# Performance work log

Hardware: AMD Instinct MI355X
Metric: run time of the kernel (lower is better)

The kernel has to match this reference:

```python
import jax, jax.numpy as jnp
import numpy as np

B, L, E, H = 2, 2048, 1024, 16
D = E // H
EPS = 1e-5


def setup_inputs() -> dict:
    key = jax.random.key(0)
    ks = jax.random.split(key, 12)
    s = 1.0 / np.sqrt(E)
    x = jax.random.normal(ks[0], (B, L, E), dtype=jnp.float32)
    # bool mask: True = block. Causal upper-triangular mask (L, S) with S == L.
    mask = jnp.triu(jnp.ones((L, L), dtype=jnp.bool_), k=1)
    Wq = jax.random.normal(ks[1], (E, E), jnp.float32) * s
    bq = jax.random.normal(ks[2], (E,), jnp.float32) * 0.01
    Wk = jax.random.normal(ks[3], (E, E), jnp.float32) * s
    bk = jax.random.normal(ks[4], (E,), jnp.float32) * 0.01
    Wv = jax.random.normal(ks[5], (E, E), jnp.float32) * s
    bv = jax.random.normal(ks[6], (E,), jnp.float32) * 0.01
    Wo = jax.random.normal(ks[7], (E, E), jnp.float32) * s
    bo = jax.random.normal(ks[8], (E,), jnp.float32) * 0.01
    gamma = jnp.ones((E,), jnp.float32)
    beta = jnp.zeros((E,), jnp.float32)
    return {"x": x, "mask": mask, "Wq": Wq, "bq": bq, "Wk": Wk, "bk": bk,
            "Wv": Wv, "bv": bv, "Wo": Wo, "bo": bo, "gamma": gamma, "beta": beta}


def reference(x, mask, Wq, bq, Wk, bk, Wv, bv, Wo, bo, gamma, beta):
    b, l, e = x.shape
    x = jnp.nan_to_num(x, nan=0.0, posinf=1e9, neginf=-1e9)
    # QKV projections (torch Linear: x @ W.T + b), split heads -> (B,H,L,D)
    q = (x @ Wq.T + bq).reshape(b, l, H, D).transpose(0, 2, 1, 3)
    k = (x @ Wk.T + bk).reshape(b, l, H, D).transpose(0, 2, 1, 3)
    v = (x @ Wv.T + bv).reshape(b, l, H, D).transpose(0, 2, 1, 3)
    scale = max(D ** 0.5, 1e-6)
    scores = jnp.einsum('bhtd,bhsd->bhts', q, k) / scale  # (B,H,L,L)
    # bool mask True=block -> additive -inf, broadcast (L,L) over (B,H)
    scores = scores + jnp.where(mask, -jnp.inf, 0.0).astype(scores.dtype)
    scores = scores - jnp.max(scores, axis=-1, keepdims=True)
    scores = jnp.nan_to_num(scores, nan=0.0, posinf=1e9, neginf=-1e9)
    attn = jax.nn.softmax(scores, axis=-1)
    o = jnp.einsum('bhts,bhsd->bhtd', attn, v)
    o = o.transpose(0, 2, 1, 3).reshape(b, l, e)
    y = o @ Wo.T + bo
    r = y + x
    # LayerNorm over last dim
    mu = jnp.mean(r, axis=-1, keepdims=True)
    var = jnp.mean((r - mu) ** 2, axis=-1, keepdims=True)
    out = (r - mu) * jax.lax.rsqrt(var + EPS) * gamma + beta
    out = jnp.nan_to_num(out, nan=0.0, posinf=1e9, neginf=-1e9)
    return out
```

## Files before the change

### kernel.cpp

```cpp
#include <hip/hip_runtime.h>
#include <hip/hip_bf16.h>
#include <cstdint>
#include <cstddef>

#define NB 2
#define NL 2048
#define NE 1024
#define NH 16
#define ND 64
#define NM (NB * NL)

typedef float f32x4 __attribute__((ext_vector_type(4)));
typedef __bf16 bf16x8 __attribute__((ext_vector_type(8)));
typedef __bf16 bf16x4 __attribute__((ext_vector_type(4)));

#define DEV static __device__ __forceinline__

DEV f32x4 mfma16(bf16x8 a, bf16x8 b, f32x4 c) {
  return __builtin_amdgcn_mfma_f32_16x16x32_bf16(a, b, c, 0, 0, 0);
}

DEV ushort f2bf(float f) {
  uint32_t u = __float_as_uint(f);
  uint32_t r = (u + 0x7fffu + ((u >> 16) & 1u)) >> 16;
  return (ushort)r;
}

#if __has_builtin(__builtin_amdgcn_exp2f)
DEV float fast_exp2(float x) { return __builtin_amdgcn_exp2f(x); }
#else
DEV float fast_exp2(float x) { return exp2f(x); }
#endif

DEV void gl_lds16(const void* src, void* lds_dst) {
  __builtin_amdgcn_global_load_lds(
      (const __attribute__((address_space(1))) void*)src,
      (__attribute__((address_space(3))) void*)lds_dst, 16, 0, 0);
}

template <int NCALLS>
DEV void stage_swz(const char* gbase, size_t row_stride_b, char* lds_base, int tid) {
#pragma unroll
  for (int c = 0; c < NCALLS; ++c) {
    uint32_t P = (uint32_t)(c * 4096 + tid * 16);
    uint32_t r = P >> 7;
    uint32_t Lo = P ^ ((r & 7u) << 4);
    gl_lds16(gbase + (size_t)r * row_stride_b + (Lo & 127u), lds_base + P);
  }
}

DEV void stage8k_swz(const char* gbase, size_t row_stride_b, char* lds_base, int tid) {
  uint32_t P = (uint32_t)(tid * 16);
  uint32_t r = P >> 7;
  uint32_t Lo = P ^ ((r & 7u) << 4);
  gl_lds16(gbase + (size_t)r * row_stride_b + (Lo & 127u), lds_base + P);
}

DEV void stage_chunk(const char* gbase, size_t row_stride_b, char* lds_base,
                     int tid, int c) {
  uint32_t P = (uint32_t)(c * 8192 + tid * 16);
  uint32_t r = P >> 7;
  uint32_t Lo = P ^ ((r & 7u) << 4);
  gl_lds16(gbase + (size_t)r * row_stride_b + (Lo & 127u), lds_base + P);
}

__global__ __launch_bounds__(256) void pack_kernel(
    const float* __restrict__ x, const float* __restrict__ wq,
    const float* __restrict__ wk, const float* __restrict__ wv,
    const float* __restrict__ wo, ushort* __restrict__ xb,
    ushort* __restrict__ wqb, ushort* __restrict__ wkb,
    ushort* __restrict__ wvb, ushort* __restrict__ wob) {
  int64_t q = (int64_t)blockIdx.x * 256 + threadIdx.x;
  const float* src;
  ushort* dst;
  bool cl;
  if (q < 1048576) {
    src = x + q * 4;
    dst = xb + q * 4;
    cl = true;
  } else {
    int64_t r = q - 1048576;
    int wsel = (int)(r >> 18);
    int64_t o = (r & 262143) * 4;
    cl = false;
    if (wsel == 0) { src = wq + o; dst = wqb + o; }
    else if (wsel == 1) { src = wk + o; dst = wkb + o; }
    else if (wsel == 2) { src = wv + o; dst = wvb + o; }
    else { src = wo + o; dst = wob + o; }
  }
  float4 v = *(const float4*)src;
  if (cl) {
    v.x = (v.x != v.x) ? 0.f : fminf(fmaxf(v.x, -1e9f), 1e9f);
    v.y = (v.y != v.y) ? 0.f : fminf(fmaxf(v.y, -1e9f), 1e9f);
    v.z = (v.z != v.z) ? 0.f : fminf(fmaxf(v.z, -1e9f), 1e9f);
    v.w = (v.w != v.w) ? 0.f : fminf(fmaxf(v.w, -1e9f), 1e9f);
  }
  ushort4 o4;
  o4.x = f2bf(v.x);
  o4.y = f2bf(v.y);
  o4.z = f2bf(v.z);
  o4.w = f2bf(v.w);
  *(ushort4*)dst = o4;
}

__global__ __launch_bounds__(512) void qkv_gemm_kernel(
    const ushort* __restrict__ xb, const ushort* __restrict__ wqkv,
    const float* __restrict__ bq, const float* __restrict__ bk,
    const float* __restrict__ bv, ushort* __restrict__ Qo,
    ushort* __restrict__ Ko, ushort* __restrict__ Vto) {
  __shared__ __align__(128) char lds[114688];
  const int tid = threadIdx.x;
  const int ln = tid & 63;
  const int ln15 = ln & 15, g = ln >> 4;
  const int wid = tid >> 6;
  const int wr = wid >> 2, wc = wid & 3;
  const int mt_ = blockIdx.x >> 4, nt_ = blockIdx.x & 15;
  const int m0 = mt_ * 256, n0 = nt_ * 192;

  const char* Abase = (const char*)xb + (size_t)m0 * 2048;
  const char* Bbase = (const char*)wqkv + (size_t)n0 * 2048;

  f32x4 acc[8][3];
#pragma unroll
  for (int mi = 0; mi < 8; ++mi)
#pragma unroll
    for (int ni = 0; ni < 3; ++ni) acc[mi][ni] = {0.f, 0.f, 0.f, 0.f};

  stage_chunk(Abase, 2048, lds, tid, 0);
  stage_chunk(Abase, 2048, lds, tid, 1);
  stage_chunk(Abase, 2048, lds, tid, 2);
  stage_chunk(Abase, 2048, lds, tid, 3);
  stage_chunk(Bbase, 2048, lds + 65536, tid, 0);
  stage_chunk(Bbase, 2048, lds + 65536, tid, 1);
  stage_chunk(Bbase, 2048, lds + 65536, tid, 2);

  for (int kt = 0; kt < 16; ++kt) {
    asm volatile("s_waitcnt vmcnt(0)" ::: "memory");
    __builtin_amdgcn_s_barrier();
    asm volatile("" ::: "memory");
    const char* ab = lds + (kt & 1) * 32768;
    const char* bb = lds + 65536 + (kt & 1) * 24576;
    const char* anx = Abase + (kt + 1) * 128;
    const char* bnx = Bbase + (kt + 1) * 128;
    char* a_dst = lds + ((kt + 1) & 1) * 32768;
    char* b_dst = lds + 65536 + ((kt + 1) & 1) * 24576;

    bf16x8 bfr[2][3];
#pragma unroll
    for (int kc = 0; kc < 2; ++kc)
#pragma unroll
      for (int ni = 0; ni < 3; ++ni) {
        uint32_t br = (uint32_t)(wc * 48 + ni * 16 + ln15);
        uint32_t off = (br * 128u + (uint32_t)(kc * 64 + g * 16)) ^ ((br & 7u) << 4);
        bfr[kc][ni] = *(const bf16x8*)(bb + off);
      }
    bf16x8 afA[2][2], afB[2][2];
#pragma unroll
    for (int mi2 = 0; mi2 < 2; ++mi2)
#pragma unroll
      for (int kc = 0; kc < 2; ++kc) {
        uint32_t ar = (uint32_t)(wr * 128 + mi2 * 16 + ln15);
        uint32_t off = (ar * 128u + (uint32_t)(kc * 64 + g * 16)) ^ ((ar & 7u) << 4);
        afA[mi2][kc] = *(const bf16x8*)(ab + off);
      }

#pragma unroll
    for (int p = 0; p < 4; ++p) {
      if (kt + 1 < 16) {
        if (p == 0) { stage_chunk(anx, 2048, a_dst, tid, 0);
                      stage_chunk(anx, 2048, a_dst, tid, 1); }
        else if (p == 1) { stage_chunk(anx, 2048, a_dst, tid, 2);
                           stage_chunk(anx, 2048, a_dst, tid, 3); }
        else if (p == 2) { stage_chunk(bnx, 2048, b_dst, tid, 0);
                           stage_chunk(bnx, 2048, b_dst, tid, 1); }
        else { stage_chunk(bnx, 2048, b_dst, tid, 2); }
      }
      if (p < 3) {
#pragma unroll
        for (int mi2 = 0; mi2 < 2; ++mi2)
#pragma unroll
          for (int kc = 0; kc < 2; ++kc) {
            uint32_t ar = (uint32_t)(wr * 128 + (2 * (p + 1) + mi2) * 16 + ln15);
            uint32_t off = (ar * 128u + (uint32_t)(kc * 64 + g * 16)) ^
                           ((ar & 7u) << 4);
            if (p & 1) afA[mi2][kc] = *(const bf16x8*)(ab + off);
            else       afB[mi2][kc] = *(const bf16x8*)(ab + off);
          }
        asm volatile("s_waitcnt lgkmcnt(4)" ::: "memory");
      } else {
        asm volatile("s_waitcnt lgkmcnt(0)" ::: "memory");
      }
      __builtin_amdgcn_sched_barrier(0);
      __builtin_amdgcn_s_setprio(1);
#pragma unroll
      for (int ni = 0; ni < 3; ++ni)
#pragma unroll
        for (int kc = 0; kc < 2; ++kc)
#pragma unroll
          for (int mi2 = 0; mi2 < 2; ++mi2) {
            if (p & 1)
              acc[2 * p + mi2][ni] = mfma16(afB[mi2][kc], bfr[kc][ni],
                                            acc[2 * p + mi2][ni]);
            else
              acc[2 * p + mi2][ni] = mfma16(afA[mi2][kc], bfr[kc][ni],
                                            acc[2 * p + mi2][ni]);
          }
      __builtin_amdgcn_s_setprio(0);
    }
  }

#pragma unroll
  for (int ni = 0; ni < 3; ++ni) {
    const int col = n0 + wc * 48 + ni * 16 + ln15;
    const int which = col >> 10;
    const int cw = col & 1023;
    const int h = cw >> 6, d = cw & 63;
    const float bc = (which == 0) ? bq[cw] : (which == 1) ? bk[cw] : bv[cw];
    const float sc = (which == 0) ? 0.18033688011112042f : 1.0f;
#pragma unroll
    for (int mi = 0; mi < 8; ++mi) {
      if (which < 2) {
        ushort* dst = (which == 0) ? Qo : Ko;
#pragma unroll
        for (int j = 0; j < 4; ++j) {
          int mg = m0 + wr * 128 + mi * 16 + g * 4 + j;
          int b = mg >> 11, l = mg & 2047;
          dst[((size_t)(b * NH + h) * NL + l) * ND + d] =
              f2bf((acc[mi][ni][j] + bc) * sc);
        }
      } else {
        int mg0 = m0 + wr * 128 + mi * 16 + g * 4;
        int b = mg0 >> 11, l0 = mg0 & 2047;
        ushort4 pk;
        pk.x = f2bf(acc[mi][ni][0] + bc);
        pk.y = f2bf(acc[mi][ni][1] + bc);
        pk.z = f2bf(acc[mi][ni][2] + bc);
        pk.w = f2bf(acc[mi][ni][3] + bc);
        *(ushort4*)(Vto + ((size_t)(b * NH + h) * ND + d) * NL + l0) = pk;
      }
    }
  }
}

__global__ __launch_bounds__(512) void attn_kernel(
    const ushort* __restrict__ Q, const ushort* __restrict__ K,
    const ushort* __restrict__ Vt, ushort* __restrict__ Op) {
  __shared__ __align__(128) char lds[49152];
  const int tid = threadIdx.x;
  const int w = tid >> 6, ln = tid & 63;
  const int ln15 = ln & 15, g = ln >> 4;
  const int bx = blockIdx.x;
  const int bh = bx & 31;
  const int seg = bx >> 5;
  const int qt = (seg < 8) ? 15 - seg : seg - 8;
  const int nt = 2 * qt + 2;

  const int b = bh >> 4, h = bh & 15;
  const ushort* Qh = Q + (size_t)bh * NL * ND;
  const ushort* Kh = K + (size_t)bh * NL * ND;
  const ushort* Vth = Vt + (size_t)bh * ND * NL;
  const uint32_t pbase = 32768u + (uint32_t)w * 2048u;

  const int q0 = qt * 128;
  const int r0 = q0 + w * 16;

  bf16x8 qf[2];
#pragma unroll
  for (int kc = 0; kc < 2; ++kc)
    qf[kc] = *(const bf16x8*)(Qh + (size_t)(r0 + ln15) * ND + kc * 32 + g * 8);

  f32x4 o_acc[4];
#pragma unroll
  for (int n = 0; n < 4; ++n) o_acc[n] = {0.f, 0.f, 0.f, 0.f};
  float m_run = -1e30f, l_run = 0.f;

  int cur = 0;
  stage8k_swz((const char*)Kh, 128, lds, tid);
  stage8k_swz((const char*)Vth, (size_t)NL * 2, lds + 16384, tid);

  for (int t = 0; t < nt; ++t) {
    const int s0 = t * 64;
    asm volatile("s_waitcnt vmcnt(0)" ::: "memory");
    __builtin_amdgcn_s_barrier();
    asm volatile("" ::: "memory");
    if (t + 1 < nt) {
      stage8k_swz((const char*)Kh + (size_t)(s0 + 64) * 128, 128,
                  lds + (cur ^ 1) * 8192, tid);
      stage8k_swz((const char*)Vth + (size_t)(s0 + 64) * 2, (size_t)NL * 2,
                  lds + 16384 + (cur ^ 1) * 8192, tid);
    }

    if (s0 <= r0 + 15) {
      const char* kb = lds + cur * 8192;
      const char* vb = lds + 16384 + cur * 8192;

      f32x4 s_acc[4];
#pragma unroll
      for (int n = 0; n < 4; ++n) s_acc[n] = {0.f, 0.f, 0.f, 0.f};
      __builtin_amdgcn_s_setprio(1);
#pragma unroll
      for (int kc = 0; kc < 2; ++kc) {
        bf16x8 kf[4];
#pragma unroll
        for (int n = 0; n < 4; ++n) {
          uint32_t kr = (uint32_t)(n * 16 + ln15);
          uint32_t off = (kr * 128u + (uint32_t)(kc * 64 + g * 16)) ^ ((kr & 7u) << 4);
          kf[n] = *(const bf16x8*)(kb + off);
        }
#pragma unroll
        for (int n = 0; n < 4; ++n) s_acc[n] = mfma16(kf[n], qf[kc], s_acc[n]);
      }
      __builtin_amdgcn_s_setprio(0);

      if (s0 + 63 > r0) {
        const int qi = r0 + ln15;
#pragma unroll
        for (int n = 0; n < 4; ++n)
#pragma unroll
          for (int j = 0; j < 4; ++j) {
            int si = s0 + n * 16 + g * 4 + j;
            s_acc[n][j] = (si > qi) ? -1e30f : s_acc[n][j];
          }
      }

      float mx;
      {
        float a0 = fmaxf(fmaxf(s_acc[0][0], s_acc[0][1]), s_acc[0][2]);
        float a1 = fmaxf(fmaxf(s_acc[0][3], s_acc[1][0]), s_acc[1][1]);
        float a2 = fmaxf(fmaxf(s_acc[1][2], s_acc[1][3]), s_acc[2][0]);
        float a3 = fmaxf(fmaxf(s_acc[2][1], s_acc[2][2]), s_acc[2][3]);
        float a4 = fmaxf(fmaxf(s_acc[3][0], s_acc[3][1]), s_acc[3][2]);
        float b0 = fmaxf(fmaxf(a0, a1), a2);
        float b1 = fmaxf(fmaxf(a3, a4), s_acc[3][3]);
        mx = fmaxf(b0, b1);
      }
      if (__any(mx > m_run + 8.0f)) {
        float mr = fmaxf(mx, __shfl_xor(mx, 16));
        mr = fmaxf(mr, __shfl_xor(mr, 32));
        float mn = fmaxf(m_run, mr);
        float al = fast_exp2(m_run - mn);
        m_run = mn;
        l_run *= al;
#pragma unroll
        for (int j = 0; j < 4; ++j) {
          float aj = __shfl(al, g * 4 + j);
#pragma unroll
          for (int n = 0; n < 4; ++n) o_acc[n][j] *= aj;
        }
      }
      float ps = 0.f;
#pragma unroll
      for (int n = 0; n < 4; ++n) {
        float p0 = fast_exp2(s_acc[n][0] - m_run);
        float p1 = fast_exp2(s_acc[n][1] - m_run);
        float p2 = fast_exp2(s_acc[n][2] - m_run);
        float p3 = fast_exp2(s_acc[n][3] - m_run);
        ps += (p0 + p1) + (p2 + p3);
        bf16x4 pk = {(__bf16)p0, (__bf16)p1, (__bf16)p2, (__bf16)p3};
        uint32_t off = ((uint32_t)ln15 * 128u + (uint32_t)(n * 32 + g * 8)) ^
                       (((uint32_t)ln15 & 7u) << 4);
        *(bf16x4*)(lds + pbase + off) = pk;
      }
      l_run += ps;

      __builtin_amdgcn_s_setprio(1);
#pragma unroll
      for (int kc = 0; kc < 2; ++kc) {
        uint32_t poff = ((uint32_t)ln15 * 128u + (uint32_t)(kc * 64 + g * 16)) ^
                        (((uint32_t)ln15 & 7u) << 4);
        bf16x8 pf = *(const bf16x8*)(lds + pbase + poff);
        bf16x8 vf[4];
#pragma unroll
        for (int n = 0; n < 4; ++n) {
          uint32_t vr = (uint32_t)(n * 16 + ln15);
          uint32_t off = (vr * 128u + (uint32_t)(kc * 64 + g * 16)) ^ ((vr & 7u) << 4);
          vf[n] = *(const bf16x8*)(vb + off);
        }
#pragma unroll
        for (int n = 0; n < 4; ++n) o_acc[n] = mfma16(pf, vf[n], o_acc[n]);
      }
      __builtin_amdgcn_s_setprio(0);
    }
    cur ^= 1;
  }

  l_run += __shfl_xor(l_run, 16);
  l_run += __shfl_xor(l_run, 32);

  float invl = 1.0f / l_run;
#pragma unroll
  for (int j = 0; j < 4; ++j) {
    float inv = __shfl(invl, g * 4 + j);
    int qi = r0 + g * 4 + j;
    size_t rowo = ((size_t)b * NL + qi) * NE + h * ND;
#pragma unroll
    for (int n = 0; n < 4; ++n) Op[rowo + n * 16 + ln15] = f2bf(o_acc[n][j] * inv);
  }
}

__global__ __launch_bounds__(256) void oproj_kernel(
    const ushort* __restrict__ ob, const ushort* __restrict__ wob,
    const float* __restrict__ bo, const float* __restrict__ x,
    float* __restrict__ out) {
  __shared__ __align__(128) char lds[65536];
  const int tid = threadIdx.x;
  const int w = tid >> 6, ln = tid & 63;
  const int ln15 = ln & 15, g = ln >> 4;
  const int wm = w >> 1, wn = w & 1;
  const int m0 = blockIdx.y * 128;
  const int n0 = blockIdx.x * 128;

  const char* Abase = (const char*)ob + (size_t)m0 * 2048;
  const char* Bbase = (const char*)wob + (size_t)n0 * 2048;

  f32x4 acc[4][4];
#pragma unroll
  for (int m = 0; m < 4; ++m)
#pragma unroll
    for (int n = 0; n < 4; ++n) acc[m][n] = {0.f, 0.f, 0.f, 0.f};

  int cur = 0;
  stage_swz<4>(Abase, 2048, lds, tid);
  stage_swz<4>(Bbase, 2048, lds + 32768, tid);

  for (int kt = 0; kt < 16; ++kt) {
    asm volatile("s_waitcnt vmcnt(0)" ::: "memory");
    __builtin_amdgcn_s_barrier();
    asm volatile("" ::: "memory");
    if (kt + 1 < 16) {
      stage_swz<4>(Abase + (kt + 1) * 128, 2048, lds + (cur ^ 1) * 16384, tid);
      stage_swz<4>(Bbase + (kt + 1) * 128, 2048,
                   lds + 32768 + (cur ^ 1) * 16384, tid);
    }
    const char* ab = lds + cur * 16384;
    const char* bb = lds + 32768 + cur * 16384;
    __builtin_amdgcn_s_setprio(1);
#pragma unroll
    for (int kc = 0; kc < 2; ++kc) {
      bf16x8 af[4], bfr[4];
#pragma unroll
      for (int i = 0; i < 4; ++i) {
        uint32_t ar = (uint32_t)(wm * 64 + i * 16 + ln15);
        uint32_t ao = (ar * 128u + (uint32_t)(kc * 64 + g * 16)) ^ ((ar & 7u) << 4);
        af[i] = *(const bf16x8*)(ab + ao);
        uint32_t br = (uint32_t)(wn * 64 + i * 16 + ln15);
        uint32_t bo_ = (br * 128u + (uint32_t)(kc * 64 + g * 16)) ^ ((br & 7u) << 4);
        bfr[i] = *(const bf16x8*)(bb + bo_);
      }
#pragma unroll
      for (int m = 0; m < 4; ++m)
#pragma unroll
        for (int n = 0; n < 4; ++n) acc[m][n] = mfma16(af[m], bfr[n], acc[m][n]);
    }
    __builtin_amdgcn_s_setprio(0);
    cur ^= 1;
  }

#pragma unroll
  for (int n = 0; n < 4; ++n) {
    const int col = n0 + wn * 64 + n * 16 + ln15;
    const float bc = bo[col];
#pragma unroll
    for (int m = 0; m < 4; ++m)
#pragma unroll
      for (int j = 0; j < 4; ++j) {
        int mg = m0 + wm * 64 + m * 16 + g * 4 + j;
        size_t idx = (size_t)mg * NE + col;
        out[idx] = acc[m][n][j] + bc + x[idx];
      }
  }
}

__global__ __launch_bounds__(256) void ln_kernel(float* __restrict__ io,
                                                 const float* __restrict__ gamma,
                                                 const float* __restrict__ beta) {
  const int row = blockIdx.x, tid = threadIdx.x;
  const int w = tid >> 6, ln = tid & 63;
  float4 v = *(const float4*)(io + (size_t)row * NE + tid * 4);
  float s = v.x + v.y + v.z + v.w;
  float ss = v.x * v.x + v.y * v.y + v.z * v.z + v.w * v.w;
#pragma unroll
  for (int d = 1; d < 64; d <<= 1) {
    s += __shfl_xor(s, d);
    ss += __shfl_xor(ss, d);
  }
  __shared__ float red[8];
  if (ln == 0) {
    red[w] = s;
    red[4 + w] = ss;
  }
  __syncthreads();
  s = red[0] + red[1] + red[2] + red[3];
  ss = red[4] + red[5] + red[6] + red[7];
  const float mu = s * (1.0f / (float)NE);
  float var = ss * (1.0f / (float)NE) - mu * mu;
  const float inv = rsqrtf(var + 1e-5f);
  float4 gv = *(const float4*)(gamma + tid * 4);
  float4 bv = *(const float4*)(beta + tid * 4);
  float4 o;
  o.x = (v.x - mu) * inv * gv.x + bv.x;
  o.y = (v.y - mu) * inv * gv.y + bv.y;
  o.z = (v.z - mu) * inv * gv.z + bv.z;
  o.w = (v.w - mu) * inv * gv.w + bv.w;
  *(float4*)(io + (size_t)row * NE + tid * 4) = o;
}

extern "C" void kernel_launch(void* const* d_in, const int* in_sizes, int n_in,
                              void* d_out, int out_size, void* d_ws, size_t ws_size,
                              hipStream_t stream) {
  const float* x = (const float*)d_in[0];
  const float* Wq = (const float*)d_in[2];
  const float* bq = (const float*)d_in[3];
  const float* Wk = (const float*)d_in[4];
  const float* bk = (const float*)d_in[5];
  const float* Wv = (const float*)d_in[6];
  const float* bv = (const float*)d_in[7];
  const float* Wo = (const float*)d_in[8];
  const float* bo = (const float*)d_in[9];
  const float* gamma = (const float*)d_in[10];
  const float* beta = (const float*)d_in[11];

  char* ws = (char*)d_ws;
  ushort* xb  = (ushort*)(ws + 0);
  ushort* wqb = (ushort*)(ws + 8388608);
  ushort* wkb = (ushort*)(ws + 10485760);
  ushort* wvb = (ushort*)(ws + 12582912);
  ushort* wob = (ushort*)(ws + 14680064);
  ushort* Qb  = (ushort*)(ws + 16777216);
  ushort* Kb  = (ushort*)(ws + 25165824);
  ushort* Vtb = (ushort*)(ws + 33554432);
  ushort* Ob  = (ushort*)(ws + 41943040);

  pack_kernel<<<8192, 256, 0, stream>>>(x, Wq, Wk, Wv, Wo, xb, wqb, wkb, wvb, wob);
  qkv_gemm_kernel<<<256, 512, 0, stream>>>(xb, wqb, bq, bk, bv, Qb, Kb, Vtb);
  attn_kernel<<<512, 512, 0, stream>>>(Qb, Kb, Vtb, Ob);
  oproj_kernel<<<dim3(8, 32), 256, 0, stream>>>(Ob, wob, bo, x, (float*)d_out);
  ln_kernel<<<4096, 256, 0, stream>>>((float*)d_out, gamma, beta);
}
```

Measured before the change: 103.4 us.

## Switch QKV GEMM to 32x32x16 MFMA with 4x2 wave tiling

Rewrites the QKV projection GEMM inner loop to use 32x32x16 bf16 MFMA instead of 16x16x32. Wave layout changes from 2x4 (128x48 per wave) to 4x2 (64x96 per wave), and the LDS fragment loads and epilogue indexing are adjusted to match. The goal is fewer MFMA issues and LDS fragment reads per FLOP, using larger accumulators. The trade-off is a different LDS read pattern and a shallower prefetch depth that may expose latency.

```diff
diff --git a/kernel.cpp b/kernel.cpp
--- a/kernel.cpp
+++ b/kernel.cpp
@@ -11,6 +11,7 @@
 #define NM (NB * NL)
 
 typedef float f32x4 __attribute__((ext_vector_type(4)));
+typedef float f32x16 __attribute__((ext_vector_type(16)));
 typedef __bf16 bf16x8 __attribute__((ext_vector_type(8)));
 typedef __bf16 bf16x4 __attribute__((ext_vector_type(4)));
 
@@ -18,6 +19,10 @@
 
 DEV f32x4 mfma16(bf16x8 a, bf16x8 b, f32x4 c) {
   return __builtin_amdgcn_mfma_f32_16x16x32_bf16(a, b, c, 0, 0, 0);
+}
+
+DEV f32x16 mfma32(bf16x8 a, bf16x8 b, f32x16 c) {
+  return __builtin_amdgcn_mfma_f32_32x32x16_bf16(a, b, c, 0, 0, 0);
 }
 
 DEV ushort f2bf(float f) {
@@ -111,20 +116,21 @@
   __shared__ __align__(128) char lds[114688];
   const int tid = threadIdx.x;
   const int ln = tid & 63;
-  const int ln15 = ln & 15, g = ln >> 4;
+  const int l31 = ln & 31, hi = ln >> 5;
   const int wid = tid >> 6;
-  const int wr = wid >> 2, wc = wid & 3;
-  const int mt_ = blockIdx.x >> 4, nt_ = blockIdx.x & 15;
-  const int m0 = mt_ * 256, n0 = nt_ * 192;
+  const int wr = wid >> 1, wc = wid & 1;
+  const int m0 = (blockIdx.x >> 4) * 256, n0 = (blockIdx.x & 15) * 192;
 
   const char* Abase = (const char*)xb + (size_t)m0 * 2048;
   const char* Bbase = (const char*)wqkv + (size_t)n0 * 2048;
 
-  f32x4 acc[8][3];
-#pragma unroll
-  for (int mi = 0; mi < 8; ++mi)
-#pragma unroll
-    for (int ni = 0; ni < 3; ++ni) acc[mi][ni] = {0.f, 0.f, 0.f, 0.f};
+  f32x16 acc[2][3];
+#pragma unroll
+  for (int mi = 0; mi < 2; ++mi)
+#pragma unroll
+    for (int ni = 0; ni < 3; ++ni)
+#pragma unroll
+      for (int e = 0; e < 16; ++e) acc[mi][ni][e] = 0.f;
 
   stage_chunk(Abase, 2048, lds, tid, 0);
   stage_chunk(Abase, 2048, lds, tid, 1);
@@ -145,24 +151,19 @@
     char* a_dst = lds + ((kt + 1) & 1) * 32768;
     char* b_dst = lds + 65536 + ((kt + 1) & 1) * 24576;
 
-    bf16x8 bfr[2][3];
-#pragma unroll
-    for (int kc = 0; kc < 2; ++kc)
-#pragma unroll
-      for (int ni = 0; ni < 3; ++ni) {
-        uint32_t br = (uint32_t)(wc * 48 + ni * 16 + ln15);
-        uint32_t off = (br * 128u + (uint32_t)(kc * 64 + g * 16)) ^ ((br & 7u) << 4);
-        bfr[kc][ni] = *(const bf16x8*)(bb + off);
-      }
-    bf16x8 afA[2][2], afB[2][2];
-#pragma unroll
-    for (int mi2 = 0; mi2 < 2; ++mi2)
-#pragma unroll
-      for (int kc = 0; kc < 2; ++kc) {
-        uint32_t ar = (uint32_t)(wr * 128 + mi2 * 16 + ln15);
-        uint32_t off = (ar * 128u + (uint32_t)(kc * 64 + g * 16)) ^ ((ar & 7u) << 4);
-        afA[mi2][kc] = *(const bf16x8*)(ab + off);
-      }
+    bf16x8 aF[2][2], bF[2][3];
+#pragma unroll
+    for (int mi = 0; mi < 2; ++mi) {
+      uint32_t ar = (uint32_t)(wr * 64 + mi * 32 + l31);
+      uint32_t off = (ar * 128u + (uint32_t)(hi * 16)) ^ ((ar & 7u) << 4);
+      aF[0][mi] = *(const bf16x8*)(ab + off);
+    }
+#pragma unroll
+    for (int ni = 0; ni < 3; ++ni) {
+      uint32_t br = (uint32_t)(wc * 96 + ni * 32 + l31);
+      uint32_t off = (br * 128u + (uint32_t)(hi * 16)) ^ ((br & 7u) << 4);
+      bF[0][ni] = *(const bf16x8*)(bb + off);
+    }
 
 #pragma unroll
     for (int p = 0; p < 4; ++p) {
@@ -176,17 +177,22 @@
         else { stage_chunk(bnx, 2048, b_dst, tid, 2); }
       }
       if (p < 3) {
-#pragma unroll
-        for (int mi2 = 0; mi2 < 2; ++mi2)
-#pragma unroll
-          for (int kc = 0; kc < 2; ++kc) {
-            uint32_t ar = (uint32_t)(wr * 128 + (2 * (p + 1) + mi2) * 16 + ln15);
-            uint32_t off = (ar * 128u + (uint32_t)(kc * 64 + g * 16)) ^
-                           ((ar & 7u) << 4);
-            if (p & 1) afA[mi2][kc] = *(const bf16x8*)(ab + off);
-            else       afB[mi2][kc] = *(const bf16x8*)(ab + off);
-          }
-        asm volatile("s_waitcnt lgkmcnt(4)" ::: "memory");
+        const int kc = p + 1;
+#pragma unroll
+        for (int mi = 0; mi < 2; ++mi) {
+          uint32_t ar = (uint32_t)(wr * 64 + mi * 32 + l31);
+          uint32_t off = (ar * 128u + (uint32_t)(kc * 32 + hi * 16)) ^
+                         ((ar & 7u) << 4);
+          aF[(p + 1) & 1][mi] = *(const bf16x8*)(ab + off);
+        }
+#pragma unroll
+        for (int ni = 0; ni < 3; ++ni) {
+          uint32_t br = (uint32_t)(wc * 96 + ni * 32 + l31);
+          uint32_t off = (br * 128u + (uint32_t)(kc * 32 + hi * 16)) ^
+                         ((br & 7u) << 4);
+          bF[(p + 1) & 1][ni] = *(const bf16x8*)(bb + off);
+        }
+        asm volatile("s_waitcnt lgkmcnt(5)" ::: "memory");
       } else {
         asm volatile("s_waitcnt lgkmcnt(0)" ::: "memory");
       }
@@ -195,48 +201,40 @@
 #pragma unroll
       for (int ni = 0; ni < 3; ++ni)
 #pragma unroll
-        for (int kc = 0; kc < 2; ++kc)
-#pragma unroll
-          for (int mi2 = 0; mi2 < 2; ++mi2) {
-            if (p & 1)
-              acc[2 * p + mi2][ni] = mfma16(afB[mi2][kc], bfr[kc][ni],
-                                            acc[2 * p + mi2][ni]);
-            else
-              acc[2 * p + mi2][ni] = mfma16(afA[mi2][kc], bfr[kc][ni],
-                                            acc[2 * p + mi2][ni]);
-          }
+        for (int mi = 0; mi < 2; ++mi)
+          acc[mi][ni] = mfma32(aF[p & 1][mi], bF[p & 1][ni], acc[mi][ni]);
       __builtin_amdgcn_s_setprio(0);
     }
   }
 
 #pragma unroll
   for (int ni = 0; ni < 3; ++ni) {
-    const int col = n0 + wc * 48 + ni * 16 + ln15;
+    const int col = n0 + wc * 96 + ni * 32 + l31;
     const int which = col >> 10;
     const int cw = col & 1023;
     const int h = cw >> 6, d = cw & 63;
     const float bc = (which == 0) ? bq[cw] : (which == 1) ? bk[cw] : bv[cw];
     const float sc = (which == 0) ? 0.18033688011112042f : 1.0f;
 #pragma unroll
-    for (int mi = 0; mi < 8; ++mi) {
-      if (which < 2) {
-        ushort* dst = (which == 0) ? Qo : Ko;
-#pragma unroll
-        for (int j = 0; j < 4; ++j) {
-          int mg = m0 + wr * 128 + mi * 16 + g * 4 + j;
-          int b = mg >> 11, l = mg & 2047;
-          dst[((size_t)(b * NH + h) * NL + l) * ND + d] =
-              f2bf((acc[mi][ni][j] + bc) * sc);
+    for (int mi = 0; mi < 2; ++mi) {
+#pragma unroll
+      for (int rq = 0; rq < 4; ++rq) {
+        const int mg0 = m0 + wr * 64 + mi * 32 + rq * 8 + hi * 4;
+        const int b = mg0 >> 11, l0 = mg0 & 2047;
+        if (which < 2) {
+          ushort* dst = (which == 0) ? Qo : Ko;
+#pragma unroll
+          for (int j = 0; j < 4; ++j)
+            dst[((size_t)(b * NH + h) * NL + (l0 + j)) * ND + d] =
+                f2bf((acc[mi][ni][rq * 4 + j] + bc) * sc);
+        } else {
+          ushort4 pk;
+          pk.x = f2bf(acc[mi][ni][rq * 4 + 0] + bc);
+          pk.y = f2bf(acc[mi][ni][rq * 4 + 1] + bc);
+          pk.z = f2bf(acc[mi][ni][rq * 4 + 2] + bc);
+          pk.w = f2bf(acc[mi][ni][rq * 4 + 3] + bc);
+          *(ushort4*)(Vto + ((size_t)(b * NH + h) * ND + d) * NL + l0) = pk;
         }
-      } else {
-        int mg0 = m0 + wr * 128 + mi * 16 + g * 4;
-        int b = mg0 >> 11, l0 = mg0 & 2047;
-        ushort4 pk;
-        pk.x = f2bf(acc[mi][ni][0] + bc);
-        pk.y = f2bf(acc[mi][ni][1] + bc);
-        pk.z = f2bf(acc[mi][ni][2] + bc);
-        pk.w = f2bf(acc[mi][ni][3] + bc);
-        *(ushort4*)(Vto + ((size_t)(b * NH + h) * ND + d) * NL + l0) = pk;
       }
     }
   }
```

New measurement: 105.0 us. About the same (+1.5%).
